# Performance work log

Hardware: AMD Instinct MI355X
Metric: run time of the kernel (lower is better)

## Reference

```python
import jax, jax.numpy as jnp
import numpy as np
from jax import lax

B, C_E, C_D, H, W, K = 64, 768, 512, 28, 28, 3
EPS = 1e-6


def setup_inputs() -> dict:
    key = jax.random.key(0)
    k1, k2, k3, k4, k5 = jax.random.split(key, 5)
    bcff = jax.random.normal(k1, (B, C_E, H, W), dtype=jnp.float32)
    cur_active = jax.random.bernoulli(k2, p=0.25, shape=(B, 1, H, W))
    # learned mask token, trunc-normal(std=0.02)
    mask_token = jnp.clip(0.02 * jax.random.normal(k3, (1, C_E, 1, 1), dtype=jnp.float32), -0.02, 0.02)
    ln_weight = jnp.ones((C_E,), dtype=jnp.float32)
    ln_bias = jnp.zeros((C_E,), dtype=jnp.float32)
    fan_in = C_E * K * K
    bound = 1.0 / np.sqrt(fan_in)
    conv_w = jax.random.uniform(k4, (C_D, C_E, K, K), minval=-bound, maxval=bound, dtype=jnp.float32)
    conv_b = jax.random.uniform(k5, (C_D,), minval=-bound, maxval=bound, dtype=jnp.float32)
    return {"bcff": bcff, "cur_active": cur_active, "mask_token": mask_token,
            "ln_weight": ln_weight, "ln_bias": ln_bias, "conv_w": conv_w, "conv_b": conv_b}


def reference(bcff, cur_active, mask_token, ln_weight, ln_bias, conv_w, conv_b):
    # Sparse channels-first LayerNorm: per-position LN over C. Original gathers
    # active positions, LNs them, scatters back into zeros. Since inactive
    # positions are subsequently replaced by mask tokens via torch.where, the
    # dense-LN-then-where form below is mathematically identical.
    mu = jnp.mean(bcff, axis=1, keepdims=True)                      # [B,1,H,W]
    var = jnp.mean((bcff - mu) ** 2, axis=1, keepdims=True)         # biased var, like torch LN
    normed = (bcff - mu) * lax.rsqrt(var + EPS)
    normed = ln_weight[None, :, None, None] * normed + ln_bias[None, :, None, None]
    # masked token fill: active positions keep normed features, inactive get mask token
    x = jnp.where(cur_active, normed, mask_token)                   # [B,C_E,H,W]
    # densify_proj: 3x3 conv, stride 1, padding 1, with bias
    y = lax.conv_general_dilated(x, conv_w, window_strides=(1, 1), padding="SAME",
                                 dimension_numbers=("NCHW", "OIHW", "NCHW"))
    return y + conv_b[None, :, None, None]
```

## Files before the change

kernel.cpp:

```cpp
#include <hip/hip_runtime.h>
#include <cstdint>
#include <cstddef>

#define CE 768
#define CD 512
#define NB 64
#define HH 28
#define WW 28
#define HP 30
#define WP 30
#define POS 784
#define M_TOT 50176
#define K_TOT 6912
#define MP 57600
#define XP_PIX 57728

typedef _Float16 f16x8 __attribute__((ext_vector_type(8)));
typedef _Float16 f16x4 __attribute__((ext_vector_type(4)));
typedef float f32x4 __attribute__((ext_vector_type(4)));

__global__ void prep_w_kernel(const float* __restrict__ cw, _Float16* __restrict__ wT) {
  __shared__ _Float16 s[K_TOT];
  int co = blockIdx.x;
  const float4* src4 = (const float4*)(cw + (size_t)co * K_TOT);
  for (int j = threadIdx.x; j < K_TOT / 4; j += 256) {
    float4 v = src4[j];
    f16x4 o = { (_Float16)v.x, (_Float16)v.y, (_Float16)v.z, (_Float16)v.w };
    *(f16x4*)&s[j * 4] = o;
  }
  __syncthreads();
  _Float16* dst = wT + (size_t)co * K_TOT;
  for (int j4 = threadIdx.x; j4 < K_TOT / 4; j4 += 256) {
    int tap = j4 / 192;
    int ci0 = (j4 - tap * 192) * 4;
    f16x4 o = { s[(ci0 + 0) * 9 + tap], s[(ci0 + 1) * 9 + tap],
                s[(ci0 + 2) * 9 + tap], s[(ci0 + 3) * 9 + tap] };
    *(f16x4*)&dst[j4 * 4] = o;
  }
}

__global__ void __launch_bounds__(512) ln_fused_kernel(
    const float* __restrict__ bcff, const int* __restrict__ act,
    const float* __restrict__ mtok, const float* __restrict__ gamma,
    const float* __restrict__ beta, _Float16* __restrict__ xp) {
  int b = blockIdx.x / HP, ph = blockIdx.x % HP;
  _Float16* xrow = xp + ((size_t)(b * HP + ph)) * WP * CE;
  const int tid = threadIdx.x;
  if (ph == 0 || ph == HP - 1) {
    uint4* p = (uint4*)xrow;
    uint4 z = make_uint4(0, 0, 0, 0);
    for (int j = tid; j < (WP * CE * 2) / 16; j += 512) p[j] = z;
    return;
  }
  int h = ph - 1;
  {
    uint4 z = make_uint4(0, 0, 0, 0);
    uint4* p0 = (uint4*)xrow;
    uint4* p1 = (uint4*)(xrow + (size_t)(WP - 1) * CE);
    for (int j = tid; j < (CE * 2) / 16; j += 512) { p0[j] = z; p1[j] = z; }
  }

  __shared__ _Float16 tile[WW][776];
  __shared__ float s_gamma[CE], s_beta[CE];
  __shared__ _Float16 s_mt[CE];
  __shared__ float s_mean[WW], s_rstd[WW];
  __shared__ int s_act[WW];

  for (int c = tid; c < CE; c += 512) {
    s_gamma[c] = gamma[c];
    s_beta[c] = beta[c];
    s_mt[c] = (_Float16)mtok[c];
  }
  if (tid < WW) s_act[tid] = act[b * POS + h * WW + tid];

  const float4* src4 = (const float4*)(bcff + ((size_t)b * CE * HH + h) * WW);
  for (int i = tid; i < 1344; i += 512) {
    int cq = i / 7, w4 = i - cq * 7;
    int c0 = cq * 4;
    float4 v0 = src4[(size_t)(c0 + 0) * 196 + w4];
    float4 v1 = src4[(size_t)(c0 + 1) * 196 + w4];
    float4 v2 = src4[(size_t)(c0 + 2) * 196 + w4];
    float4 v3 = src4[(size_t)(c0 + 3) * 196 + w4];
    f16x4 o0 = { (_Float16)v0.x, (_Float16)v1.x, (_Float16)v2.x, (_Float16)v3.x };
    f16x4 o1 = { (_Float16)v0.y, (_Float16)v1.y, (_Float16)v2.y, (_Float16)v3.y };
    f16x4 o2 = { (_Float16)v0.z, (_Float16)v1.z, (_Float16)v2.z, (_Float16)v3.z };
    f16x4 o3 = { (_Float16)v0.w, (_Float16)v1.w, (_Float16)v2.w, (_Float16)v3.w };
    *(f16x4*)&tile[w4 * 4 + 0][c0] = o0;
    *(f16x4*)&tile[w4 * 4 + 1][c0] = o1;
    *(f16x4*)&tile[w4 * 4 + 2][c0] = o2;
    *(f16x4*)&tile[w4 * 4 + 3][c0] = o3;
  }
  __syncthreads();

  if (tid < WW * 16) {
    int w = tid >> 4, j = tid & 15;
    float s = 0.f, ss = 0.f;
    const _Float16* row = &tile[w][j * 48];
#pragma unroll
    for (int k = 0; k < 6; ++k) {
      f16x8 v = *(const f16x8*)(row + k * 8);
#pragma unroll
      for (int u = 0; u < 8; ++u) { float f = (float)v[u]; s += f; ss += f * f; }
    }
#pragma unroll
    for (int d = 8; d; d >>= 1) {
      s += __shfl_down(s, d, 16);
      ss += __shfl_down(ss, d, 16);
    }
    if (j == 0) {
      float mu = s * (1.f / 768.f);
      float var = ss * (1.f / 768.f) - mu * mu;
      s_mean[w] = mu;
      s_rstd[w] = rsqrtf(var + 1e-6f);
    }
  }
  __syncthreads();

  for (int i = tid; i < WW * 96; i += 512) {
    int w = i / 96, q = i - w * 96;
    int c0 = q * 8;
    f16x8 o;
    if (s_act[w]) {
      f16x8 v = *(const f16x8*)&tile[w][c0];
      float mu = s_mean[w], rs = s_rstd[w];
#pragma unroll
      for (int u = 0; u < 8; ++u)
        o[u] = (_Float16)(((float)v[u] - mu) * rs * s_gamma[c0 + u] + s_beta[c0 + u]);
    } else {
      o = *(const f16x8*)&s_mt[c0];
    }
    *(f16x8*)(xrow + (size_t)(w + 1) * CE + c0) = o;
  }
}

#define GLDS(src, dst) __builtin_amdgcn_global_load_lds( \
    (const __attribute__((address_space(1))) void*)(src), \
    (__attribute__((address_space(3))) void*)(dst), 16, 0, 0)

__global__ void __launch_bounds__(512) conv_strip_kernel(
    const _Float16* __restrict__ xp, const _Float16* __restrict__ wT,
    const float* __restrict__ bias, float* __restrict__ out) {
  __shared__ _Float16 smem[24576];
  char* sAb = (char*)smem;
  char* sBb = sAb + 12288;

  const int t = threadIdx.x;
  const int lane = t & 63, wv = t >> 6;
  const int nb = blockIdx.x & 7;
  const int mb = blockIdx.x >> 3;
  const int p0 = mb * 128;
  const int n0 = nb * 64;

  const int jj = (t & 3) ^ ((t >> 3) & 3);
  const int pixA = t >> 2;
  const _Float16* pA0 = xp + (size_t)(p0 + pixA) * CE + jj * 8;
  const _Float16* pA1 = pA0 + (size_t)128 * CE;
  const int rowB = (t >> 2) & 63;
  const int hiB = t >> 8;
  const _Float16* pB = wT + (size_t)(n0 + rowB) * K_TOT + jj * 8;
  char* dA0 = sAb + wv * 1024;
  char* dA1 = sAb + 8192 + wv * 1024;
  char* dB0 = sBb + wv * 1024;

  const int wm = wv >> 1, wn = wv & 1;
  const int rowbase0 = wm * 32 + (lane & 15);
  const int lq = lane >> 4;
  const int bfrag_off = (wn * 32 + (lane & 15)) * 64 +
                        ((lq ^ (((lane & 15) >> 1) & 3)) * 16);

  f32x4 acc[2][2] = {};
  const int tap_off[9] = {0, 1, 2, 30, 31, 32, 60, 61, 62};

  for (int c24 = 0; c24 < 24; ++c24) {
    const int koff = c24 * 32;
    GLDS(pA0 + koff, dA0);
    if (wv < 4) GLDS(pA1 + koff, dA1);
#pragma unroll
    for (int k = 0; k < 4; ++k)
      GLDS(pB + (2 * k + hiB) * CE + koff, dB0 + 8192 * k);
    if (wv < 4) GLDS(pB + 8 * CE + koff, dB0 + 32768);
    __syncthreads();

#pragma unroll
    for (int tap = 0; tap < 9; ++tap) {
      const int rA = rowbase0 + tap_off[tap];
      const char* aptr = sAb + rA * 64 + ((lq ^ ((rA >> 1) & 3)) * 16);
      f16x8 a0 = *(const f16x8*)(aptr);
      f16x8 a1 = *(const f16x8*)(aptr + 1024);
      const char* bptr = sBb + tap * 4096 + bfrag_off;
      f16x8 b0 = *(const f16x8*)(bptr);
      f16x8 b1 = *(const f16x8*)(bptr + 1024);
      acc[0][0] = __builtin_amdgcn_mfma_f32_16x16x32_f16(a0, b0, acc[0][0], 0, 0, 0);
      acc[0][1] = __builtin_amdgcn_mfma_f32_16x16x32_f16(a0, b1, acc[0][1], 0, 0, 0);
      acc[1][0] = __builtin_amdgcn_mfma_f32_16x16x32_f16(a1, b0, acc[1][0], 0, 0, 0);
      acc[1][1] = __builtin_amdgcn_mfma_f32_16x16x32_f16(a1, b1, acc[1][1], 0, 0, 0);
    }
    __syncthreads();
  }

  float bv[2];
#pragma unroll
  for (int ni = 0; ni < 2; ++ni) bv[ni] = bias[n0 + wn * 32 + ni * 16 + (lane & 15)];
#pragma unroll
  for (int mi = 0; mi < 2; ++mi) {
    int g = p0 + wm * 32 + mi * 16 + (lane >> 4) * 4;
    int b = g / 900;
    int q = g - b * 900;
    int ph = q / 30, pw = q - ph * 30;
#pragma unroll
    for (int ni = 0; ni < 2; ++ni) {
      int co = n0 + wn * 32 + ni * 16 + (lane & 15);
      f32x4 v = acc[mi][ni];
      v += bv[ni];
      float* obase = out + ((size_t)b * CD + co) * POS;
      if (b < NB && ph < 28) {
        if (pw <= 24) {
          *(f32x4*)(obase + ph * 28 + pw) = v;
        } else if (pw == 26) {
          obase[ph * 28 + 26] = v[0];
          obase[ph * 28 + 27] = v[1];
        }
      }
      if (pw == 28) {
        int b2 = b, ph2 = ph + 1;
        if (ph2 == 30) { b2++; ph2 = 0; }
        if (b2 < NB && ph2 < 28) {
          float* o2 = out + ((size_t)b2 * CD + co) * POS + ph2 * 28;
          o2[0] = v[2];
          o2[1] = v[3];
        }
      }
    }
  }
}

extern "C" void kernel_launch(void* const* d_in, const int* in_sizes, int n_in,
                              void* d_out, int out_size, void* d_ws, size_t ws_size,
                              hipStream_t stream) {
  const float* bcff = (const float*)d_in[0];
  const int* cur_active = (const int*)d_in[1];
  const float* mask_token = (const float*)d_in[2];
  const float* ln_w = (const float*)d_in[3];
  const float* ln_b = (const float*)d_in[4];
  const float* conv_w = (const float*)d_in[5];
  const float* conv_b = (const float*)d_in[6];
  float* out = (float*)d_out;

  char* ws = (char*)d_ws;
  _Float16* xp = (_Float16*)ws;
  _Float16* wT = (_Float16*)(ws + (size_t)XP_PIX * CE * 2);

  prep_w_kernel<<<dim3(CD), dim3(256), 0, stream>>>(conv_w, wT);
  ln_fused_kernel<<<dim3(NB * HP), dim3(512), 0, stream>>>(bcff, cur_active, mask_token,
                                                           ln_w, ln_b, xp);
  conv_strip_kernel<<<dim3(450 * 8), dim3(512), 0, stream>>>(xp, wT, conv_b, out);
}
```

Baseline: 663.2 us.

## Enlarge conv block tile to 256x128 with 4x4 MFMA fragments per wave

Doubles the conv output tile per block from 128 pixels x 64 channels to 256 x 128, with each wave computing a 4x4 grid of 16x16 MFMA tiles. Each staged A and B fragment now feeds more MFMAs, so there are fewer LDS reads and less global traffic per FLOP. The cost is more LDS (about 92KB), many more accumulator registers, and only 900 blocks, which lowers occupancy and may leave CUs underfilled or cause register spills.

```diff
diff --git a/kernel.cpp b/kernel.cpp
--- a/kernel.cpp
+++ b/kernel.cpp
@@ -140,76 +140,78 @@
 __global__ void __launch_bounds__(512) conv_strip_kernel(
     const _Float16* __restrict__ xp, const _Float16* __restrict__ wT,
     const float* __restrict__ bias, float* __restrict__ out) {
-  __shared__ _Float16 smem[24576];
+  __shared__ _Float16 smem[47104];
   char* sAb = (char*)smem;
-  char* sBb = sAb + 12288;
+  char* sBb = sAb + 20480;
 
   const int t = threadIdx.x;
   const int lane = t & 63, wv = t >> 6;
-  const int nb = blockIdx.x & 7;
-  const int mb = blockIdx.x >> 3;
-  const int p0 = mb * 128;
-  const int n0 = nb * 64;
+  const int nb = blockIdx.x & 3;
+  const int mb = blockIdx.x >> 2;
+  const int p0 = mb * 256;
+  const int n0 = nb * 128;
 
   const int jj = (t & 3) ^ ((t >> 3) & 3);
   const int pixA = t >> 2;
-  const _Float16* pA0 = xp + (size_t)(p0 + pixA) * CE + jj * 8;
-  const _Float16* pA1 = pA0 + (size_t)128 * CE;
-  const int rowB = (t >> 2) & 63;
-  const int hiB = t >> 8;
-  const _Float16* pB = wT + (size_t)(n0 + rowB) * K_TOT + jj * 8;
-  char* dA0 = sAb + wv * 1024;
-  char* dA1 = sAb + 8192 + wv * 1024;
-  char* dB0 = sBb + wv * 1024;
+  const _Float16* pA = xp + (size_t)(p0 + pixA) * CE + jj * 8;
+  const int colB = t >> 2;
+  const _Float16* pB = wT + (size_t)(n0 + colB) * K_TOT + jj * 8;
+  char* dA = sAb + t * 16;
+  char* dB = sBb + t * 16;
 
   const int wm = wv >> 1, wn = wv & 1;
-  const int rowbase0 = wm * 32 + (lane & 15);
   const int lq = lane >> 4;
-  const int bfrag_off = (wn * 32 + (lane & 15)) * 64 +
-                        ((lq ^ (((lane & 15) >> 1) & 3)) * 16);
-
-  f32x4 acc[2][2] = {};
+  const int l15 = lane & 15;
+  const int rowbase0 = wm * 64 + l15;
+  const int bbase = (wn * 64 + l15) * 64 + ((lq ^ ((l15 >> 1) & 3)) * 16);
+
+  f32x4 acc[4][4] = {};
   const int tap_off[9] = {0, 1, 2, 30, 31, 32, 60, 61, 62};
 
   for (int c24 = 0; c24 < 24; ++c24) {
     const int koff = c24 * 32;
-    GLDS(pA0 + koff, dA0);
-    if (wv < 4) GLDS(pA1 + koff, dA1);
-#pragma unroll
-    for (int k = 0; k < 4; ++k)
-      GLDS(pB + (2 * k + hiB) * CE + koff, dB0 + 8192 * k);
-    if (wv < 4) GLDS(pB + 8 * CE + koff, dB0 + 32768);
+    GLDS(pA + koff, dA);
+    GLDS(pA + (size_t)128 * CE + koff, dA + 8192);
+    if (t < 256) GLDS(pA + (size_t)256 * CE + koff, dA + 16384);
+#pragma unroll
+    for (int k = 0; k < 9; ++k)
+      GLDS(pB + k * CE + koff, dB + 8192 * k);
     __syncthreads();
 
 #pragma unroll
     for (int tap = 0; tap < 9; ++tap) {
       const int rA = rowbase0 + tap_off[tap];
-      const char* aptr = sAb + rA * 64 + ((lq ^ ((rA >> 1) & 3)) * 16);
-      f16x8 a0 = *(const f16x8*)(aptr);
-      f16x8 a1 = *(const f16x8*)(aptr + 1024);
-      const char* bptr = sBb + tap * 4096 + bfrag_off;
-      f16x8 b0 = *(const f16x8*)(bptr);
-      f16x8 b1 = *(const f16x8*)(bptr + 1024);
-      acc[0][0] = __builtin_amdgcn_mfma_f32_16x16x32_f16(a0, b0, acc[0][0], 0, 0, 0);
-      acc[0][1] = __builtin_amdgcn_mfma_f32_16x16x32_f16(a0, b1, acc[0][1], 0, 0, 0);
-      acc[1][0] = __builtin_amdgcn_mfma_f32_16x16x32_f16(a1, b0, acc[1][0], 0, 0, 0);
-      acc[1][1] = __builtin_amdgcn_mfma_f32_16x16x32_f16(a1, b1, acc[1][1], 0, 0, 0);
+      f16x8 a[4], b[4];
+#pragma unroll
+      for (int mi = 0; mi < 4; ++mi) {
+        const int r = rA + mi * 16;
+        a[mi] = *(const f16x8*)(sAb + r * 64 + ((lq ^ ((r >> 1) & 3)) * 16));
+      }
+      const char* bp = sBb + tap * 8192 + bbase;
+#pragma unroll
+      for (int ni = 0; ni < 4; ++ni)
+        b[ni] = *(const f16x8*)(bp + ni * 1024);
+#pragma unroll
+      for (int mi = 0; mi < 4; ++mi)
+#pragma unroll
+        for (int ni = 0; ni < 4; ++ni)
+          acc[mi][ni] = __builtin_amdgcn_mfma_f32_16x16x32_f16(a[mi], b[ni], acc[mi][ni], 0, 0, 0);
     }
     __syncthreads();
   }
 
-  float bv[2];
-#pragma unroll
-  for (int ni = 0; ni < 2; ++ni) bv[ni] = bias[n0 + wn * 32 + ni * 16 + (lane & 15)];
-#pragma unroll
-  for (int mi = 0; mi < 2; ++mi) {
-    int g = p0 + wm * 32 + mi * 16 + (lane >> 4) * 4;
+  float bv[4];
+#pragma unroll
+  for (int ni = 0; ni < 4; ++ni) bv[ni] = bias[n0 + wn * 64 + ni * 16 + l15];
+#pragma unroll
+  for (int mi = 0; mi < 4; ++mi) {
+    int g = p0 + wm * 64 + mi * 16 + lq * 4;
     int b = g / 900;
     int q = g - b * 900;
     int ph = q / 30, pw = q - ph * 30;
 #pragma unroll
-    for (int ni = 0; ni < 2; ++ni) {
-      int co = n0 + wn * 32 + ni * 16 + (lane & 15);
+    for (int ni = 0; ni < 4; ++ni) {
+      int co = n0 + wn * 64 + ni * 16 + l15;
       f32x4 v = acc[mi][ni];
       v += bv[ni];
       float* obase = out + ((size_t)b * CD + co) * POS;
@@ -253,5 +255,5 @@
   prep_w_kernel<<<dim3(CD), dim3(256), 0, stream>>>(conv_w, wT);
   ln_fused_kernel<<<dim3(NB * HP), dim3(512), 0, stream>>>(bcff, cur_active, mask_token,
                                                            ln_w, ln_b, xp);
-  conv_strip_kernel<<<dim3(450 * 8), dim3(512), 0, stream>>>(xp, wT, conv_b, out);
-}
+  conv_strip_kernel<<<dim3(225 * 4), dim3(512), 0, stream>>>(xp, wT, conv_b, out);
+}
```

New measurement: 704.1 us. 6.2% more time.
